# Performance work log

Hardware: AMD Instinct MI355X
Metric: run time of the kernel (lower is better)

Reference implementation:

```python
import jax, jax.numpy as jnp
import numpy as np

INPUT_DIM = 512
D_KQ = 64
D_V = 64
SEQ = 8192


def setup_inputs() -> dict:
    key = jax.random.key(0)
    k_x, k_q, k_k, k_v = jax.random.split(key, 4)
    x = jax.random.normal(k_x, (SEQ, INPUT_DIM), dtype=jnp.float32)
    # Original uses torch.rand (uniform [0,1)) for the parameters.
    W_query = jax.random.uniform(k_q, (INPUT_DIM, D_KQ), dtype=jnp.float32)
    W_key = jax.random.uniform(k_k, (INPUT_DIM, D_KQ), dtype=jnp.float32)
    W_value = jax.random.uniform(k_v, (INPUT_DIM, D_V), dtype=jnp.float32)
    return {"x": x, "W_query": W_query, "W_key": W_key, "W_value": W_value}


def reference(x, W_query, W_key, W_value):
    # Full-recompute path of AttentionOptimized: single-head attention.
    Q = x @ W_query          # [T, d_kq]
    K = x @ W_key            # [T, d_kq]
    V = x @ W_value          # [T, d_v]
    scale = jnp.asarray(D_KQ, x.dtype) ** 0.5
    scores = Q @ K.T         # [T, T]
    attn = jax.nn.softmax(scores / scale, axis=-1)
    return attn @ V          # [T, d_v]
```

## Files before the change

kernel.cpp:

```cpp
#include <hip/hip_runtime.h>
#include <hip/hip_bf16.h>
#include <math.h>

#define SEQ 8192
#define DIN 512
#define DH  64
#define SG  16
#define CHUNK (SEQ / SG)
#define BK  64
#define NIT (CHUNK / BK)
#define LDK 64
#define SXP 516

typedef float f32x4 __attribute__((ext_vector_type(4)));
typedef short short8 __attribute__((ext_vector_type(8)));
typedef ushort us4 __attribute__((ext_vector_type(4)));

static __device__ __forceinline__ ushort bf16_of(float v) {
  __hip_bfloat16 h = __float2bfloat16(v);
  return *reinterpret_cast<ushort*>(&h);
}
static __device__ __forceinline__ float f_of_bf16(ushort u) {
  __hip_bfloat16 h;
  *reinterpret_cast<ushort*>(&h) = u;
  return __bfloat162float(h);
}
static __device__ __forceinline__ f32x4 mfma16(short8 a, short8 b, f32x4 c) {
  return __builtin_amdgcn_mfma_f32_16x16x32_bf16(a, b, c, 0, 0, 0);
}
static __device__ __forceinline__ uint pack_bf16(float a, float b) {
  __hip_bfloat162 h2 = __float22bfloat162_rn(make_float2(a, b));
  return *reinterpret_cast<uint*>(&h2);
}
static __device__ __forceinline__ int slot_of(int p) {
  return ((((p >> 2) & 1) * 2 + (p >> 5)) << 4) | (((p >> 3) & 3) << 2) | (p & 3);
}
static __device__ __forceinline__ int swz(int row, int col) {
  return col ^ ((row & 7) << 3);
}

__global__ __launch_bounds__(256, 2) void pgemm_kernel(
    const float* __restrict__ x,  const float* __restrict__ Wq,
    const float* __restrict__ Wk, const float* __restrict__ Wv,
    ushort* __restrict__ Qh, ushort* __restrict__ Ql,
    ushort* __restrict__ Kh, ushort* __restrict__ Kl,
    ushort* __restrict__ Vt) {
  __shared__ float sx[16][SXP];
  float* mb = &sx[0][0];

  const int tid = threadIdx.x;
  const int wv = tid >> 6, lane = tid & 63;
  const int ln = lane & 15, qd = lane >> 4;
  const int rb = blockIdx.x * 16;

  {
    const float4* xg = reinterpret_cast<const float4*>(x + (size_t)rb * DIN);
#pragma unroll
    for (int j = 0; j < 8; ++j) {
      const int idx = tid + 256 * j;
      const int row = idx >> 7;
      const int col = (idx & 127) * 4;
      *reinterpret_cast<float4*>(&sx[row][col]) = xg[idx];
    }
  }
  __syncthreads();

  f32x4 acc[3][4];
#pragma unroll
  for (int m = 0; m < 3; ++m)
#pragma unroll
    for (int nt = 0; nt < 4; ++nt)
#pragma unroll
      for (int i = 0; i < 4; ++i) acc[m][nt][i] = 0.f;

  const int kb = wv * 128;
  const int wbase = (kb + qd * 8) * 64 + ln;

  float wf[2][32];
#define LDW(kt_, m_, buf_)                                                     \
  do {                                                                         \
    const float* W_ = ((m_) == 0) ? Wq : (((m_) == 1) ? Wk : Wv);              \
    const int o_ = wbase + (kt_) * 32 * 64;                                    \
    _Pragma("unroll") for (int nt = 0; nt < 4; ++nt)                           \
      _Pragma("unroll") for (int j = 0; j < 8; ++j)                            \
        wf[buf_][nt * 8 + j] = W_[o_ + j * 64 + nt * 16];                      \
  } while (0)

  LDW(0, 0, 0);
#pragma unroll
  for (int kt = 0; kt < 4; ++kt) {
    const int k0 = kb + kt * 32;
    float xs[8];
    *reinterpret_cast<float4*>(xs) =
        *reinterpret_cast<const float4*>(&sx[ln][k0 + qd * 8]);
    *reinterpret_cast<float4*>(xs + 4) =
        *reinterpret_cast<const float4*>(&sx[ln][k0 + qd * 8 + 4]);
    ushort ah[8] __attribute__((aligned(16)));
    ushort al[8] __attribute__((aligned(16)));
#pragma unroll
    for (int j = 0; j < 8; ++j) {
      const ushort h = bf16_of(xs[j]);
      ah[j] = h;
      al[j] = bf16_of(xs[j] - f_of_bf16(h));
    }
    const short8 Ah = *reinterpret_cast<short8*>(ah);
    const short8 Al = *reinterpret_cast<short8*>(al);
#pragma unroll
    for (int m = 0; m < 3; ++m) {
      const int g = kt * 3 + m;
      const int buf = g & 1;
      if (g < 11) {
        const int gn = g + 1;
        LDW(gn / 3, gn % 3, buf ^ 1);
      }
      const float scale = (m == 0) ? 0.125f * 1.44269504088896f : 1.0f;
#pragma unroll
      for (int nt = 0; nt < 4; ++nt) {
        ushort bh8[8] __attribute__((aligned(16)));
        ushort bl8[8] __attribute__((aligned(16)));
#pragma unroll
        for (int j = 0; j < 8; ++j) {
          const float v = wf[buf][nt * 8 + j] * scale;
          const ushort h = bf16_of(v);
          bh8[j] = h;
          bl8[j] = bf16_of(v - f_of_bf16(h));
        }
        const short8 bh = *reinterpret_cast<short8*>(bh8);
        const short8 bl = *reinterpret_cast<short8*>(bl8);
        acc[m][nt] = mfma16(Ah, bh, acc[m][nt]);
        acc[m][nt] = mfma16(Ah, bl, acc[m][nt]);
        acc[m][nt] = mfma16(Al, bh, acc[m][nt]);
      }
    }
  }
#undef LDW

  const int eidx = (qd * 4) * 64 + ln;
  __syncthreads();
  if (wv >= 2) {
    float* b = mb + (size_t)(wv - 2) * 3072;
#pragma unroll
    for (int m = 0; m < 3; ++m)
#pragma unroll
      for (int nt = 0; nt < 4; ++nt)
#pragma unroll
        for (int r = 0; r < 4; ++r)
          b[m * 1024 + eidx + r * 64 + nt * 16] = acc[m][nt][r];
  }
  __syncthreads();
  if (wv < 2) {
    const float* b = mb + (size_t)wv * 3072;
#pragma unroll
    for (int m = 0; m < 3; ++m)
#pragma unroll
      for (int nt = 0; nt < 4; ++nt)
#pragma unroll
        for (int r = 0; r < 4; ++r)
          acc[m][nt][r] += b[m * 1024 + eidx + r * 64 + nt * 16];
  }
  __syncthreads();
  if (wv == 1) {
#pragma unroll
    for (int m = 0; m < 3; ++m)
#pragma unroll
      for (int nt = 0; nt < 4; ++nt)
#pragma unroll
        for (int r = 0; r < 4; ++r)
          mb[m * 1024 + eidx + r * 64 + nt * 16] = acc[m][nt][r];
  }
  __syncthreads();
  if (wv == 0) {
#pragma unroll
    for (int m = 0; m < 3; ++m)
#pragma unroll
      for (int nt = 0; nt < 4; ++nt)
#pragma unroll
        for (int r = 0; r < 4; ++r)
          acc[m][nt][r] += mb[m * 1024 + eidx + r * 64 + nt * 16];

#pragma unroll
    for (int m = 0; m < 2; ++m) {
      ushort* H = (m == 0) ? Qh : Kh;
      ushort* L = (m == 0) ? Ql : Kl;
#pragma unroll
      for (int nt = 0; nt < 4; ++nt)
#pragma unroll
        for (int r = 0; r < 4; ++r) {
          const float v = acc[m][nt][r];
          const int row = rb + qd * 4 + r;
          const int col = nt * 16 + ln;
          const ushort h = bf16_of(v);
          H[(size_t)row * DH + col] = h;
          L[(size_t)row * DH + col] = bf16_of(v - f_of_bf16(h));
        }
    }
#pragma unroll
    for (int nt = 0; nt < 4; ++nt) {
      ushort vp[4] __attribute__((aligned(8)));
#pragma unroll
      for (int r = 0; r < 4; ++r) vp[r] = bf16_of(acc[2][nt][r]);
      *reinterpret_cast<us4*>(Vt + (size_t)(nt * 16 + ln) * SEQ + rb + qd * 4) =
          *reinterpret_cast<us4*>(vp);
    }
  }
}

__global__ __launch_bounds__(256, 3) void flash_kernel(
    const ushort* __restrict__ Qh, const ushort* __restrict__ Ql,
    const ushort* __restrict__ Kh, const ushort* __restrict__ Kl,
    const ushort* __restrict__ Vt,
    ushort* __restrict__ Opart, float* __restrict__ Mpart,
    float* __restrict__ Lpart) {
  __shared__ __attribute__((aligned(16))) ushort sKh[2][BK][LDK];
  __shared__ __attribute__((aligned(16))) ushort sKl[2][BK][LDK];
  __shared__ __attribute__((aligned(16))) ushort sVt[2][DH][LDK];

  const int tid  = threadIdx.x;
  const int wv   = tid >> 6;
  const int lane = tid & 63;
  const int ln   = lane & 15;
  const int qd   = lane >> 4;
  const int bid  = blockIdx.x;
  const int sg   = bid & (SG - 1);
  const int qt   = bid / SG;
  const int qrow0  = qt * 128 + wv * 32;
  const int k0base = sg * CHUNK;

  const int r0 = tid >> 3, g0 = (tid & 7) * 8;
  const int r1 = r0 + 32,  g1 = g0;
  const int sr0 = slot_of(r0), sr1 = slot_of(r1);

  const ushort one_u = (ln == 0) ? (ushort)0x3F80 : (ushort)0;
  short8 afr1;
#pragma unroll
  for (int j = 0; j < 8; ++j) afr1[j] = (short)one_u;

  short8 bqh[2][2], bql[2][2];
#pragma unroll
  for (int s = 0; s < 2; ++s)
#pragma unroll
    for (int kt = 0; kt < 2; ++kt) {
      bqh[s][kt] = *reinterpret_cast<const short8*>(
          Qh + (size_t)(qrow0 + s * 16 + ln) * DH + kt * 32 + qd * 8);
      bql[s][kt] = *reinterpret_cast<const short8*>(
          Ql + (size_t)(qrow0 + s * 16 + ln) * DH + kt * 32 + qd * 8);
    }

  f32x4 accO[2][4], accL[2];
  float m_run[2] = {-INFINITY, -INFINITY};
#pragma unroll
  for (int s = 0; s < 2; ++s) {
#pragma unroll
    for (int nt = 0; nt < 4; ++nt)
#pragma unroll
      for (int i = 0; i < 4; ++i) accO[s][nt][i] = 0.f;
#pragma unroll
    for (int i = 0; i < 4; ++i) accL[s][i] = 0.f;
  }

  uint4 pk0, pk1, pl0, pl1, pv0, pv1;
#define LOAD_TILES(k0_)                                                        \
  do {                                                                         \
    pk0 = *reinterpret_cast<const uint4*>(Kh + (size_t)((k0_) + r0) * DH + g0);\
    pk1 = *reinterpret_cast<const uint4*>(Kh + (size_t)((k0_) + r1) * DH + g1);\
    pl0 = *reinterpret_cast<const uint4*>(Kl + (size_t)((k0_) + r0) * DH + g0);\
    pl1 = *reinterpret_cast<const uint4*>(Kl + (size_t)((k0_) + r1) * DH + g1);\
    pv0 = *reinterpret_cast<const uint4*>(Vt + (size_t)r0 * SEQ + (k0_) + g0); \
    pv1 = *reinterpret_cast<const uint4*>(Vt + (size_t)r1 * SEQ + (k0_) + g1); \
  } while (0)
#define STORE_TILES(b_)                                                        \
  do {                                                                         \
    *reinterpret_cast<uint4*>(&sKh[b_][sr0][swz(sr0, g0)]) = pk0;              \
    *reinterpret_cast<uint4*>(&sKh[b_][sr1][swz(sr1, g1)]) = pk1;              \
    *reinterpret_cast<uint4*>(&sKl[b_][sr0][swz(sr0, g0)]) = pl0;              \
    *reinterpret_cast<uint4*>(&sKl[b_][sr1][swz(sr1, g1)]) = pl1;              \
    *reinterpret_cast<uint4*>(&sVt[b_][r0][swz(r0, g0)])   = pv0;              \
    *reinterpret_cast<uint4*>(&sVt[b_][r1][swz(r1, g1)])   = pv1;              \
  } while (0)

  LOAD_TILES(k0base);
  STORE_TILES(0);
  __syncthreads();

  for (int it = 0; it < NIT; ++it) {
    const int cur = it & 1;
    const int k0n = k0base + ((it + 1 < NIT) ? (it + 1) : it) * BK;
    LOAD_TILES(k0n);

    f32x4 accS[2][4];
#pragma unroll
    for (int nt = 0; nt < 4; ++nt) {
#pragma unroll
      for (int s = 0; s < 2; ++s)
#pragma unroll
        for (int i = 0; i < 4; ++i) accS[s][nt][i] = 0.f;
      const int kr = nt * 16 + ln;
      const short8 kh0 = *reinterpret_cast<const short8*>(&sKh[cur][kr][swz(kr, qd * 8)]);
      const short8 kh1 = *reinterpret_cast<const short8*>(&sKh[cur][kr][swz(kr, 32 + qd * 8)]);
      const short8 kl0 = *reinterpret_cast<const short8*>(&sKl[cur][kr][swz(kr, qd * 8)]);
      const short8 kl1 = *reinterpret_cast<const short8*>(&sKl[cur][kr][swz(kr, 32 + qd * 8)]);
#pragma unroll
      for (int s = 0; s < 2; ++s) {
        accS[s][nt] = mfma16(kh0, bqh[s][0], accS[s][nt]);
        accS[s][nt] = mfma16(kh1, bqh[s][1], accS[s][nt]);
        accS[s][nt] = mfma16(kh0, bql[s][0], accS[s][nt]);
        accS[s][nt] = mfma16(kh1, bql[s][1], accS[s][nt]);
        accS[s][nt] = mfma16(kl0, bqh[s][0], accS[s][nt]);
        accS[s][nt] = mfma16(kl1, bqh[s][1], accS[s][nt]);
      }
    }

    uint pkd[2][4][2];
#pragma unroll
    for (int s = 0; s < 2; ++s) {
      float tmax = fmaxf(
          fmaxf(fmaxf(accS[s][0][0], accS[s][0][1]), fmaxf(accS[s][0][2], accS[s][0][3])),
          fmaxf(fmaxf(accS[s][1][0], accS[s][1][1]), fmaxf(accS[s][1][2], accS[s][1][3])));
      tmax = fmaxf(tmax, fmaxf(
          fmaxf(fmaxf(accS[s][2][0], accS[s][2][1]), fmaxf(accS[s][2][2], accS[s][2][3])),
          fmaxf(fmaxf(accS[s][3][0], accS[s][3][1]), fmaxf(accS[s][3][2], accS[s][3][3]))));
      tmax = fmaxf(tmax, __shfl_xor(tmax, 16));
      tmax = fmaxf(tmax, __shfl_xor(tmax, 32));
      const float mnew  = fmaxf(m_run[s], tmax);
      const float alpha = exp2f(m_run[s] - mnew);
      m_run[s] = mnew;
#pragma unroll
      for (int nt = 0; nt < 4; ++nt) {
        const float p0 = exp2f(accS[s][nt][0] - mnew);
        const float p1 = exp2f(accS[s][nt][1] - mnew);
        const float p2 = exp2f(accS[s][nt][2] - mnew);
        const float p3 = exp2f(accS[s][nt][3] - mnew);
        pkd[s][nt][0] = pack_bf16(p0, p1);
        pkd[s][nt][1] = pack_bf16(p2, p3);
#pragma unroll
        for (int i = 0; i < 4; ++i) accO[s][nt][i] *= alpha;
      }
      accL[s][0] *= alpha;
    }

#pragma unroll
    for (int kt2 = 0; kt2 < 2; ++kt2) {
      short8 pfrag[2];
#pragma unroll
      for (int s = 0; s < 2; ++s) {
        uint4 du;
        du.x = pkd[s][kt2][0];
        du.y = pkd[s][kt2][1];
        du.z = pkd[s][kt2 + 2][0];
        du.w = pkd[s][kt2 + 2][1];
        pfrag[s] = *reinterpret_cast<short8*>(&du);
      }
#pragma unroll
      for (int nt2 = 0; nt2 < 4; ++nt2) {
        const int vr = nt2 * 16 + ln;
        const short8 vA = *reinterpret_cast<const short8*>(
            &sVt[cur][vr][swz(vr, kt2 * 32 + qd * 8)]);
        accO[0][nt2] = mfma16(vA, pfrag[0], accO[0][nt2]);
        accO[1][nt2] = mfma16(vA, pfrag[1], accO[1][nt2]);
      }
      accL[0] = mfma16(afr1, pfrag[0], accL[0]);
      accL[1] = mfma16(afr1, pfrag[1], accL[1]);
    }

    if (it + 1 < NIT) {
      STORE_TILES(cur ^ 1);
      __syncthreads();
    }
  }
#undef LOAD_TILES
#undef STORE_TILES

#pragma unroll
  for (int s = 0; s < 2; ++s) {
    const int qrow = qrow0 + s * 16 + ln;
    ushort* Ob = Opart + ((size_t)sg * SEQ + qrow) * DH;
#pragma unroll
    for (int nt = 0; nt < 4; ++nt) {
      ushort op[4] __attribute__((aligned(8)));
#pragma unroll
      for (int r = 0; r < 4; ++r) op[r] = bf16_of(accO[s][nt][r]);
      *reinterpret_cast<us4*>(Ob + nt * 16 + qd * 4) =
          *reinterpret_cast<us4*>(op);
    }
    if (qd == 0) {
      Mpart[(size_t)sg * SEQ + qrow] = m_run[s];
      Lpart[(size_t)sg * SEQ + qrow] = accL[s][0];
    }
  }
}

__global__ __launch_bounds__(256) void merge_kernel(
    const ushort* __restrict__ Opart, const float* __restrict__ Mpart,
    const float* __restrict__ Lpart, float* __restrict__ out) {
  const int idx = blockIdx.x * 256 + threadIdx.x;
  const int row = idx >> 4;
  const int c4  = (idx & 15) * 4;

  float m[SG];
  float M = -INFINITY;
#pragma unroll
  for (int i = 0; i < SG; ++i) {
    m[i] = Mpart[(size_t)i * SEQ + row];
    M = fmaxf(M, m[i]);
  }
  float L = 0.f;
  float a0 = 0.f, a1 = 0.f, a2 = 0.f, a3 = 0.f;
#pragma unroll
  for (int i = 0; i < SG; ++i) {
    const float w = exp2f(m[i] - M);
    L += w * Lpart[(size_t)i * SEQ + row];
    const us4 o = *reinterpret_cast<const us4*>(
        Opart + ((size_t)i * SEQ + row) * DH + c4);
    a0 += w * f_of_bf16(o[0]);
    a1 += w * f_of_bf16(o[1]);
    a2 += w * f_of_bf16(o[2]);
    a3 += w * f_of_bf16(o[3]);
  }
  const float rL = 1.0f / L;
  float4 res = make_float4(a0 * rL, a1 * rL, a2 * rL, a3 * rL);
  *reinterpret_cast<float4*>(out + (size_t)row * DH + c4) = res;
}

extern "C" void kernel_launch(void* const* d_in, const int* in_sizes, int n_in,
                              void* d_out, int out_size, void* d_ws, size_t ws_size,
                              hipStream_t stream) {
  const float* x  = (const float*)d_in[0];
  const float* Wq = (const float*)d_in[1];
  const float* Wk = (const float*)d_in[2];
  const float* Wv = (const float*)d_in[3];
  float* out = (float*)d_out;

  const size_t S64 = (size_t)SEQ * DH;
  ushort* Qh = (ushort*)d_ws;
  ushort* Ql = Qh + S64;
  ushort* Kh = Ql + S64;
  ushort* Kl = Kh + S64;
  ushort* Vt = Kl + S64;
  ushort* Op = Vt + S64;
  float*  Mp = (float*)(Op + (size_t)SG * S64);
  float*  Lp = Mp + (size_t)SG * SEQ;

  pgemm_kernel<<<SEQ / 16, 256, 0, stream>>>(x, Wq, Wk, Wv, Qh, Ql, Kh, Kl, Vt);
  flash_kernel<<<(SEQ / 128) * SG, 256, 0, stream>>>(Qh, Ql, Kh, Kl, Vt, Op, Mp, Lp);
  merge_kernel<<<(SEQ * 16) / 256, 256, 0, stream>>>(Op, Mp, Lp, out);
}
```

Measured before the change: 137.9 us.

## Software-pipeline QK and softmax-PV across tiles with triple buffering, lazy rescale

Restructures the flash-attention loop so the QK^T MFMAs for the next key tile overlap the softmax and PV of the current tile, using a three-stage shared-memory ring and two score accumulator sets. The online-softmax rescale of the output now runs only when the row max grows by more than a threshold, which skips exp and multiply work on most tiles. The key split drops from 16 to 8 groups, giving fewer partials to combine and longer loops per block. Occupancy drops (launch bound 3 to 2, more LDS and registers), and exp2 values may grow to 2^8 before rescaling, which costs some bf16 precision headroom.

```diff
diff --git a/kernel.cpp b/kernel.cpp
--- a/kernel.cpp
+++ b/kernel.cpp
@@ -5,7 +5,7 @@
 #define SEQ 8192
 #define DIN 512
 #define DH  64
-#define SG  16
+#define SG  8
 #define CHUNK (SEQ / SG)
 #define BK  64
 #define NIT (CHUNK / BK)
@@ -205,15 +205,15 @@
   }
 }
 
-__global__ __launch_bounds__(256, 3) void flash_kernel(
+__global__ __launch_bounds__(256, 2) void flash_kernel(
     const ushort* __restrict__ Qh, const ushort* __restrict__ Ql,
     const ushort* __restrict__ Kh, const ushort* __restrict__ Kl,
     const ushort* __restrict__ Vt,
     ushort* __restrict__ Opart, float* __restrict__ Mpart,
     float* __restrict__ Lpart) {
-  __shared__ __attribute__((aligned(16))) ushort sKh[2][BK][LDK];
-  __shared__ __attribute__((aligned(16))) ushort sKl[2][BK][LDK];
-  __shared__ __attribute__((aligned(16))) ushort sVt[2][DH][LDK];
+  __shared__ __attribute__((aligned(16))) ushort sKh[3][BK][LDK];
+  __shared__ __attribute__((aligned(16))) ushort sKl[3][BK][LDK];
+  __shared__ __attribute__((aligned(16))) ushort sVt[3][DH][LDK];
 
   const int tid  = threadIdx.x;
   const int wv   = tid >> 6;
@@ -222,7 +222,7 @@
   const int qd   = lane >> 4;
   const int bid  = blockIdx.x;
   const int sg   = bid & (SG - 1);
-  const int qt   = bid / SG;
+  const int qt   = bid >> 3;
   const int qrow0  = qt * 128 + wv * 32;
   const int k0base = sg * CHUNK;
 
@@ -257,6 +257,9 @@
 #pragma unroll
     for (int i = 0; i < 4; ++i) accL[s][i] = 0.f;
   }
+  const f32x4 z4 = {0.f, 0.f, 0.f, 0.f};
+
+  f32x4 accSA[2][4], accSB[2][4];
 
   uint4 pk0, pk1, pl0, pl1, pv0, pv1;
 #define LOAD_TILES(k0_)                                                        \
@@ -278,95 +281,109 @@
     *reinterpret_cast<uint4*>(&sVt[b_][r1][swz(r1, g1)])   = pv1;              \
   } while (0)
 
+#define QK_PHASE(ACC, b_)                                                      \
+  do {                                                                         \
+    _Pragma("unroll") for (int nt = 0; nt < 4; ++nt) {                         \
+      const int kr = nt * 16 + ln;                                             \
+      const short8 kh0 = *reinterpret_cast<const short8*>(                     \
+          &sKh[b_][kr][swz(kr, qd * 8)]);                                      \
+      const short8 kh1 = *reinterpret_cast<const short8*>(                     \
+          &sKh[b_][kr][swz(kr, 32 + qd * 8)]);                                 \
+      const short8 kl0 = *reinterpret_cast<const short8*>(                     \
+          &sKl[b_][kr][swz(kr, qd * 8)]);                                      \
+      const short8 kl1 = *reinterpret_cast<const short8*>(                     \
+          &sKl[b_][kr][swz(kr, 32 + qd * 8)]);                                 \
+      _Pragma("unroll") for (int s = 0; s < 2; ++s) {                          \
+        ACC[s][nt] = mfma16(kh0, bqh[s][0], z4);                               \
+        ACC[s][nt] = mfma16(kh1, bqh[s][1], ACC[s][nt]);                       \
+        ACC[s][nt] = mfma16(kh0, bql[s][0], ACC[s][nt]);                       \
+        ACC[s][nt] = mfma16(kh1, bql[s][1], ACC[s][nt]);                       \
+        ACC[s][nt] = mfma16(kl0, bqh[s][0], ACC[s][nt]);                       \
+        ACC[s][nt] = mfma16(kl1, bqh[s][1], ACC[s][nt]);                       \
+      }                                                                        \
+    }                                                                          \
+  } while (0)
+
+#define SMPV_PHASE(ACC, bc_)                                                   \
+  do {                                                                         \
+    uint pkd[2][4][2];                                                         \
+    _Pragma("unroll") for (int s = 0; s < 2; ++s) {                            \
+      float tmax = fmaxf(fmaxf(ACC[s][0][0], ACC[s][0][1]), ACC[s][0][2]);     \
+      tmax = fmaxf(fmaxf(tmax, ACC[s][0][3]), ACC[s][1][0]);                   \
+      tmax = fmaxf(fmaxf(tmax, ACC[s][1][1]), ACC[s][1][2]);                   \
+      tmax = fmaxf(fmaxf(tmax, ACC[s][1][3]), ACC[s][2][0]);                   \
+      tmax = fmaxf(fmaxf(tmax, ACC[s][2][1]), ACC[s][2][2]);                   \
+      tmax = fmaxf(fmaxf(tmax, ACC[s][2][3]), ACC[s][3][0]);                   \
+      tmax = fmaxf(fmaxf(tmax, ACC[s][3][1]), ACC[s][3][2]);                   \
+      tmax = fmaxf(tmax, ACC[s][3][3]);                                        \
+      tmax = fmaxf(tmax, __shfl_xor(tmax, 16));                                \
+      tmax = fmaxf(tmax, __shfl_xor(tmax, 32));                                \
+      if (tmax > m_run[s] + 8.f) {       \
+        const float mnew  = fmaxf(m_run[s], tmax);                             \
+        const float alpha = exp2f(m_run[s] - mnew);                            \
+        m_run[s] = mnew;                                                       \
+        _Pragma("unroll") for (int nt = 0; nt < 4; ++nt)                       \
+          _Pragma("unroll") for (int i = 0; i < 4; ++i)                        \
+            accO[s][nt][i] *= alpha;                                           \
+        accL[s][0] *= alpha;                                                   \
+      }                                                                        \
+      const float mr = m_run[s];                                               \
+      _Pragma("unroll") for (int nt = 0; nt < 4; ++nt) {                       \
+        pkd[s][nt][0] = pack_bf16(exp2f(ACC[s][nt][0] - mr),                   \
+                                  exp2f(ACC[s][nt][1] - mr));                  \
+        pkd[s][nt][1] = pack_bf16(exp2f(ACC[s][nt][2] - mr),                   \
+                                  exp2f(ACC[s][nt][3] - mr));                  \
+      }                                                                        \
+    }                                                                          \
+    _Pragma("unroll") for (int kt2 = 0; kt2 < 2; ++kt2) {                      \
+      short8 pfrag[2];                                                         \
+      _Pragma("unroll") for (int s = 0; s < 2; ++s) {                          \
+        uint4 du;                                                              \
+        du.x = pkd[s][kt2][0];                                                 \
+        du.y = pkd[s][kt2][1];                                                 \
+        du.z = pkd[s][kt2 + 2][0];                                             \
+        du.w = pkd[s][kt2 + 2][1];                                             \
+        pfrag[s] = *reinterpret_cast<short8*>(&du);                            \
+      }                                                                        \
+      _Pragma("unroll") for (int nt2 = 0; nt2 < 4; ++nt2) {                    \
+        const int vr = nt2 * 16 + ln;                                          \
+        const short8 vA = *reinterpret_cast<const short8*>(                    \
+            &sVt[bc_][vr][swz(vr, kt2 * 32 + qd * 8)]);                        \
+        accO[0][nt2] = mfma16(vA, pfrag[0], accO[0][nt2]);                     \
+        accO[1][nt2] = mfma16(vA, pfrag[1], accO[1][nt2]);                     \
+      }                                                                        \
+      accL[0] = mfma16(afr1, pfrag[0], accL[0]);                               \
+      accL[1] = mfma16(afr1, pfrag[1], accL[1]);                               \
+    }                                                                          \
+  } while (0)
+
   LOAD_TILES(k0base);
   STORE_TILES(0);
-  __syncthreads();
-
-  for (int it = 0; it < NIT; ++it) {
-    const int cur = it & 1;
-    const int k0n = k0base + ((it + 1 < NIT) ? (it + 1) : it) * BK;
-    LOAD_TILES(k0n);
-
-    f32x4 accS[2][4];
-#pragma unroll
-    for (int nt = 0; nt < 4; ++nt) {
-#pragma unroll
-      for (int s = 0; s < 2; ++s)
-#pragma unroll
-        for (int i = 0; i < 4; ++i) accS[s][nt][i] = 0.f;
-      const int kr = nt * 16 + ln;
-      const short8 kh0 = *reinterpret_cast<const short8*>(&sKh[cur][kr][swz(kr, qd * 8)]);
-      const short8 kh1 = *reinterpret_cast<const short8*>(&sKh[cur][kr][swz(kr, 32 + qd * 8)]);
-      const short8 kl0 = *reinterpret_cast<const short8*>(&sKl[cur][kr][swz(kr, qd * 8)]);
-      const short8 kl1 = *reinterpret_cast<const short8*>(&sKl[cur][kr][swz(kr, 32 + qd * 8)]);
-#pragma unroll
-      for (int s = 0; s < 2; ++s) {
-        accS[s][nt] = mfma16(kh0, bqh[s][0], accS[s][nt]);
-        accS[s][nt] = mfma16(kh1, bqh[s][1], accS[s][nt]);
-        accS[s][nt] = mfma16(kh0, bql[s][0], accS[s][nt]);
-        accS[s][nt] = mfma16(kh1, bql[s][1], accS[s][nt]);
-        accS[s][nt] = mfma16(kl0, bqh[s][0], accS[s][nt]);
-        accS[s][nt] = mfma16(kl1, bqh[s][1], accS[s][nt]);
-      }
-    }
-
-    uint pkd[2][4][2];
-#pragma unroll
-    for (int s = 0; s < 2; ++s) {
-      float tmax = fmaxf(
-          fmaxf(fmaxf(accS[s][0][0], accS[s][0][1]), fmaxf(accS[s][0][2], accS[s][0][3])),
-          fmaxf(fmaxf(accS[s][1][0], accS[s][1][1]), fmaxf(accS[s][1][2], accS[s][1][3])));
-      tmax = fmaxf(tmax, fmaxf(
-          fmaxf(fmaxf(accS[s][2][0], accS[s][2][1]), fmaxf(accS[s][2][2], accS[s][2][3])),
-          fmaxf(fmaxf(accS[s][3][0], accS[s][3][1]), fmaxf(accS[s][3][2], accS[s][3][3]))));
-      tmax = fmaxf(tmax, __shfl_xor(tmax, 16));
-      tmax = fmaxf(tmax, __shfl_xor(tmax, 32));
-      const float mnew  = fmaxf(m_run[s], tmax);
-      const float alpha = exp2f(m_run[s] - mnew);
-      m_run[s] = mnew;
-#pragma unroll
-      for (int nt = 0; nt < 4; ++nt) {
-        const float p0 = exp2f(accS[s][nt][0] - mnew);
-        const float p1 = exp2f(accS[s][nt][1] - mnew);
-        const float p2 = exp2f(accS[s][nt][2] - mnew);
-        const float p3 = exp2f(accS[s][nt][3] - mnew);
-        pkd[s][nt][0] = pack_bf16(p0, p1);
-        pkd[s][nt][1] = pack_bf16(p2, p3);
-#pragma unroll
-        for (int i = 0; i < 4; ++i) accO[s][nt][i] *= alpha;
-      }
-      accL[s][0] *= alpha;
-    }
-
-#pragma unroll
-    for (int kt2 = 0; kt2 < 2; ++kt2) {
-      short8 pfrag[2];
-#pragma unroll
-      for (int s = 0; s < 2; ++s) {
-        uint4 du;
-        du.x = pkd[s][kt2][0];
-        du.y = pkd[s][kt2][1];
-        du.z = pkd[s][kt2 + 2][0];
-        du.w = pkd[s][kt2 + 2][1];
-        pfrag[s] = *reinterpret_cast<short8*>(&du);
-      }
-#pragma unroll
-      for (int nt2 = 0; nt2 < 4; ++nt2) {
-        const int vr = nt2 * 16 + ln;
-        const short8 vA = *reinterpret_cast<const short8*>(
-            &sVt[cur][vr][swz(vr, kt2 * 32 + qd * 8)]);
-        accO[0][nt2] = mfma16(vA, pfrag[0], accO[0][nt2]);
-        accO[1][nt2] = mfma16(vA, pfrag[1], accO[1][nt2]);
-      }
-      accL[0] = mfma16(afr1, pfrag[0], accL[0]);
-      accL[1] = mfma16(afr1, pfrag[1], accL[1]);
-    }
-
-    if (it + 1 < NIT) {
-      STORE_TILES(cur ^ 1);
-      __syncthreads();
-    }
-  }
+  LOAD_TILES(k0base + BK);
+  __syncthreads();
+  QK_PHASE(accSA, 0);
+  STORE_TILES(1);
+  LOAD_TILES(k0base + 2 * BK);
+  __syncthreads();
+
+  int bc = 0, bn = 1, bs = 2;
+#define BODY(ACC_CUR, ACC_NXT, t_)                                             \
+  do {                                                                         \
+    if ((t_) + 1 < NIT) QK_PHASE(ACC_NXT, bn);          \
+    SMPV_PHASE(ACC_CUR, bc);                        \
+    if ((t_) + 2 < NIT) STORE_TILES(bs);                                       \
+    if ((t_) + 3 < NIT) LOAD_TILES(k0base + ((t_) + 3) * BK);                  \
+    if ((t_) + 1 < NIT) __syncthreads();                                       \
+    const int tb_ = bc; bc = bn; bn = bs; bs = tb_;                            \
+  } while (0)
+
+  for (int t = 0; t < NIT; t += 2) {
+    BODY(accSA, accSB, t);
+    BODY(accSB, accSA, t + 1);
+  }
+#undef BODY
+#undef QK_PHASE
+#undef SMPV_PHASE
 #undef LOAD_TILES
 #undef STORE_TILES
 
```

After: 129.7 us. -6.0%, faster.
